# Kernel optimization log

Measured on AMD Instinct MI355X. Metric: run time of the kernel, lower is better.

Reference implementation:

```python
import jax, jax.numpy as jnp
import numpy as np

N = 50000   # nodes
E = 600000  # directed edges (self-loops added inside reference, per GCNConv default)
G = 64      # graphs in the batch
D = 128     # in_features
H = 128     # hidden_channels
C = 10      # num_classes


def setup_inputs() -> dict:
    key = jax.random.key(0)
    ks = jax.random.split(key, 9)
    x = jax.random.normal(ks[0], (N, D), dtype=jnp.float32)
    edge_index = jax.random.randint(ks[1], (2, E), 0, N, dtype=jnp.int64)
    batch = jnp.sort(jax.random.randint(ks[2], (N,), 0, G, dtype=jnp.int64))
    # GCNConv weights (glorot-ish scale) and biases; final linear layer
    W1 = jax.random.normal(ks[3], (D, H), dtype=jnp.float32) / np.sqrt(D).astype(np.float32)
    b1 = jnp.zeros((H,), dtype=jnp.float32)
    W2 = jax.random.normal(ks[4], (H, H), dtype=jnp.float32) / np.sqrt(H).astype(np.float32)
    b2 = jnp.zeros((H,), dtype=jnp.float32)
    Wlin = jax.random.normal(ks[5], (H, C), dtype=jnp.float32) / np.sqrt(H).astype(np.float32)
    blin = jnp.zeros((C,), dtype=jnp.float32)
    return {"x": x, "W1": W1, "b1": b1, "W2": W2, "b2": b2,
            "Wlin": Wlin, "blin": blin, "edge_index": edge_index, "batch": batch}


def _gcn_conv(x, W, b, row, col, norm):
    # x' = D^{-1/2}(A+I)D^{-1/2} (x W) + b ; aggregate messages from row (src) into col (dst)
    h = x @ W                                   # [N, H] dense GEMM
    msg = norm[:, None] * h[row]                # gather by source index [E+N, H]
    out = jax.ops.segment_sum(msg, col, num_segments=N)  # scatter-add to targets
    return out + b


def reference(x, W1, b1, W2, b2, Wlin, blin, edge_index, batch):
    loops = jnp.arange(N, dtype=edge_index.dtype)
    row = jnp.concatenate([edge_index[0], loops])   # sources (+ self loops)
    col = jnp.concatenate([edge_index[1], loops])   # targets (+ self loops)
    # symmetric degree normalization (degrees >= 1 thanks to self loops)
    deg = jax.ops.segment_sum(jnp.ones_like(col, dtype=jnp.float32), col, num_segments=N)
    dinv = jax.lax.rsqrt(deg)
    norm = dinv[row] * dinv[col]                    # [E+N]

    h = jax.nn.relu(_gcn_conv(x, W1, b1, row, col, norm))
    h = _gcn_conv(h, W2, b2, row, col, norm)

    # global mean pool over graphs
    sums = jax.ops.segment_sum(h, batch, num_segments=G)                       # [G, H]
    cnt = jax.ops.segment_sum(jnp.ones((N,), dtype=jnp.float32), batch, num_segments=G)
    pooled = sums / jnp.maximum(cnt, 1.0)[:, None]

    return pooled @ Wlin + blin                     # logits [G, C]
```

## Files before the change

kernel.cpp:

```cpp
#include <hip/hip_runtime.h>

#define NN 50000
#define NE 600000
#define NG 64
#define DIM 128
#define NCLS 10
#define SB 196
#define NNP 50176
#define KBLK 224
#define KCH 224
#define CAP 64
#define E2B ((NE / 2 + 255) / 256)

typedef unsigned short ushort;
typedef unsigned char uchar;
typedef __attribute__((ext_vector_type(8))) short short8;
typedef __attribute__((ext_vector_type(4))) float float4v;
typedef __attribute__((ext_vector_type(2))) float float2v;

__device__ __forceinline__ ushort f2bf(float f) {
    unsigned u = __float_as_uint(f);
    u += 0x7fff + ((u >> 16) & 1);
    return (ushort)(u >> 16);
}
__device__ __forceinline__ uchar f2fp8(float f) {
    int p = __builtin_amdgcn_cvt_pk_fp8_f32(f, f, 0, false);
    return (uchar)(p & 0xff);
}
__device__ __forceinline__ void accfp8(float* a, uint2 v) {
    float2v p0 = __builtin_amdgcn_cvt_pk_f32_fp8(v.x, false);
    float2v p1 = __builtin_amdgcn_cvt_pk_f32_fp8(v.x, true);
    float2v p2 = __builtin_amdgcn_cvt_pk_f32_fp8(v.y, false);
    float2v p3 = __builtin_amdgcn_cvt_pk_f32_fp8(v.y, true);
    a[0] += p0[0]; a[1] += p0[1]; a[2] += p1[0]; a[3] += p1[1];
    a[4] += p2[0]; a[5] += p2[1]; a[6] += p3[0]; a[7] += p3[1];
}

__global__ void k_init(int* __restrict__ cnt, const float* __restrict__ W1,
                       ushort* __restrict__ Wsw, float* __restrict__ Wd) {
    int b = blockIdx.x, t = threadIdx.x;
    if (b < SB) {
        int i = b * 256 + t;
        if (i < NN) cnt[i] = 0;
    } else if (b < SB + 64) {
        int tid = (b - SB) * 256 + t;
        int j = tid & 7;
        int lane = (tid >> 3) & 63;
        int frag = tid >> 9;
        int nt = frag >> 2, kc = frag & 3;
        int k = kc * 32 + (lane >> 4) * 8 + j;
        int n = nt * 16 + (lane & 15);
        Wsw[tid] = f2bf(W1[k * DIM + n]);
    } else {
        float4* w4 = (float4*)Wd;
        int base = (b - SB - 64) * 256 + t;
#pragma unroll
        for (int i = 0; i < 4; ++i)
            w4[base + i * 200704] = make_float4(0.f, 0.f, 0.f, 0.f);
    }
}

__global__ void k_fill(const int* __restrict__ row, const int* __restrict__ col,
                       int* __restrict__ cnt, int* __restrict__ ell) {
    int e = (blockIdx.x * blockDim.x + threadIdx.x) * 2;
    if (e < NE) {
        int2 r = *(const int2*)(row + e);
        int2 c = *(const int2*)(col + e);
        int p0 = atomicAdd(&cnt[c.x], 1);
        if (p0 < CAP) ell[c.x * CAP + p0] = r.x;
        int p1 = atomicAdd(&cnt[c.y], 1);
        if (p1 < CAP) ell[c.y * CAP + p1] = r.y;
    }
}

__global__ __launch_bounds__(256) void k_gemm_mfma(const float* __restrict__ Ain,
                                                   const ushort* __restrict__ Wsw,
                                                   const int* __restrict__ cnt,
                                                   uchar* __restrict__ Hs,
                                                   float* __restrict__ dinv) {
    const int t = threadIdx.x;
    const int wave = t >> 6, lane = t & 63;
    const int m = lane & 15, quad = lane >> 4;
    const int row0 = blockIdx.x * 64 + wave * 16;

    short8 bfrag[8][4];
#pragma unroll
    for (int nt = 0; nt < 8; ++nt)
#pragma unroll
        for (int kc = 0; kc < 4; ++kc)
            bfrag[nt][kc] = *(const short8*)(Wsw + ((nt * 4 + kc) * 64 + lane) * 8);

    float4v acc[8];
#pragma unroll
    for (int nt = 0; nt < 8; ++nt) acc[nt] = (float4v){0.f, 0.f, 0.f, 0.f};

    const int row = row0 + m;
    const int rclamp = row < NN ? row : NN - 1;

#pragma unroll
    for (int kc = 0; kc < 4; ++kc) {
        const float* ap = Ain + (size_t)rclamp * DIM + kc * 32 + quad * 8;
        float4 v0 = *(const float4*)ap;
        float4 v1 = *(const float4*)(ap + 4);
        union { short8 v; ushort u[8]; } tmp;
        tmp.u[0] = f2bf(v0.x); tmp.u[1] = f2bf(v0.y);
        tmp.u[2] = f2bf(v0.z); tmp.u[3] = f2bf(v0.w);
        tmp.u[4] = f2bf(v1.x); tmp.u[5] = f2bf(v1.y);
        tmp.u[6] = f2bf(v1.z); tmp.u[7] = f2bf(v1.w);
        short8 a = tmp.v;
#pragma unroll
        for (int nt = 0; nt < 8; ++nt)
            acc[nt] = __builtin_amdgcn_mfma_f32_16x16x32_bf16(a, bfrag[nt][kc], acc[nt], 0, 0, 0);
    }

#pragma unroll
    for (int reg = 0; reg < 4; ++reg) {
        int r = row0 + quad * 4 + reg;
        if (r < NN) {
            float d = rsqrtf(1.0f + (float)cnt[r]);
            if (m == 0) dinv[r] = d;
#pragma unroll
            for (int nt = 0; nt < 8; ++nt)
                Hs[(size_t)r * DIM + nt * 16 + m] = f2fp8(d * acc[nt][reg]);
        }
    }
}

__global__ __launch_bounds__(256) void k_gather_ell(const int* __restrict__ ell,
                                                    const int* __restrict__ deg,
                                                    const float* __restrict__ bias,
                                                    const uchar* __restrict__ Hs,
                                                    ushort* __restrict__ out) {
    int gt = blockIdx.x * blockDim.x + threadIdx.x;
    int node = gt >> 4, lane = gt & 15;
    if (node >= NN) return;
    const int* rowp = ell + node * CAP;
    int end = min(deg[node], CAP);
    const size_t off = (size_t)lane * 8;

    float a[8] = {0.f, 0.f, 0.f, 0.f, 0.f, 0.f, 0.f, 0.f};
    accfp8(a, *(const uint2*)(Hs + (size_t)node * DIM + off));

    int e = 0;
    for (; e + 8 <= end; e += 8) {
        int r0 = rowp[e], r1 = rowp[e + 1], r2 = rowp[e + 2], r3 = rowp[e + 3];
        int r4 = rowp[e + 4], r5 = rowp[e + 5], r6 = rowp[e + 6], r7 = rowp[e + 7];
        uint2 v0 = *(const uint2*)(Hs + (size_t)r0 * DIM + off);
        uint2 v1 = *(const uint2*)(Hs + (size_t)r1 * DIM + off);
        uint2 v2 = *(const uint2*)(Hs + (size_t)r2 * DIM + off);
        uint2 v3 = *(const uint2*)(Hs + (size_t)r3 * DIM + off);
        uint2 v4 = *(const uint2*)(Hs + (size_t)r4 * DIM + off);
        uint2 v5 = *(const uint2*)(Hs + (size_t)r5 * DIM + off);
        uint2 v6 = *(const uint2*)(Hs + (size_t)r6 * DIM + off);
        uint2 v7 = *(const uint2*)(Hs + (size_t)r7 * DIM + off);
        accfp8(a, v0); accfp8(a, v1); accfp8(a, v2); accfp8(a, v3);
        accfp8(a, v4); accfp8(a, v5); accfp8(a, v6); accfp8(a, v7);
    }
    for (; e + 4 <= end; e += 4) {
        int r0 = rowp[e], r1 = rowp[e + 1], r2 = rowp[e + 2], r3 = rowp[e + 3];
        uint2 v0 = *(const uint2*)(Hs + (size_t)r0 * DIM + off);
        uint2 v1 = *(const uint2*)(Hs + (size_t)r1 * DIM + off);
        uint2 v2 = *(const uint2*)(Hs + (size_t)r2 * DIM + off);
        uint2 v3 = *(const uint2*)(Hs + (size_t)r3 * DIM + off);
        accfp8(a, v0); accfp8(a, v1); accfp8(a, v2); accfp8(a, v3);
    }
    for (; e < end; ++e)
        accfp8(a, *(const uint2*)(Hs + (size_t)rowp[e] * DIM + off));

    float d = rsqrtf(1.0f + (float)end);
    float4 b0 = *(const float4*)(bias + off);
    float4 b1 = *(const float4*)(bias + off + 4);
    a[0] = fmaxf(fmaf(a[0], d, b0.x), 0.f); a[1] = fmaxf(fmaf(a[1], d, b0.y), 0.f);
    a[2] = fmaxf(fmaf(a[2], d, b0.z), 0.f); a[3] = fmaxf(fmaf(a[3], d, b0.w), 0.f);
    a[4] = fmaxf(fmaf(a[4], d, b1.x), 0.f); a[5] = fmaxf(fmaf(a[5], d, b1.y), 0.f);
    a[6] = fmaxf(fmaf(a[6], d, b1.z), 0.f); a[7] = fmaxf(fmaf(a[7], d, b1.w), 0.f);
    uint4 o;
    o.x = (unsigned)f2bf(a[0]) | ((unsigned)f2bf(a[1]) << 16);
    o.y = (unsigned)f2bf(a[2]) | ((unsigned)f2bf(a[3]) << 16);
    o.z = (unsigned)f2bf(a[4]) | ((unsigned)f2bf(a[5]) << 16);
    o.w = (unsigned)f2bf(a[6]) | ((unsigned)f2bf(a[7]) << 16);
    *(uint4*)(out + (size_t)node * DIM + off) = o;
}

__global__ void k_wbuild(const int* __restrict__ row, const int* __restrict__ col,
                         const float* __restrict__ dinv, const int* __restrict__ batch,
                         float* __restrict__ Wd) {
    int b = blockIdx.x, t = threadIdx.x;
    if (b < E2B) {
        int e = (b * 256 + t) * 2;
        if (e < NE) {
            int2 r = *(const int2*)(row + e);
            int2 c = *(const int2*)(col + e);
            atomicAdd(&Wd[(size_t)batch[c.x] * NNP + r.x], dinv[c.x] * dinv[r.x]);
            atomicAdd(&Wd[(size_t)batch[c.y] * NNP + r.y], dinv[c.y] * dinv[r.y]);
        }
    } else {
        int n = (b - E2B) * 256 + t;
        if (n < NN) {
            float d = dinv[n];
            atomicAdd(&Wd[(size_t)batch[n] * NNP + n], d * d);
        }
    }
}

__global__ __launch_bounds__(256) void k_pool_gemm(const float* __restrict__ Wd,
                                                   const ushort* __restrict__ A2,
                                                   float* __restrict__ partial) {
    const int t = threadIdx.x;
    const int wave = t >> 6, lane = t & 63;
    const int m = lane & 15, quad = lane >> 4;
    const int g = wave * 16 + m;
    const size_t k0 = (size_t)blockIdx.x * KCH;

    float4v acc[8];
#pragma unroll
    for (int nt = 0; nt < 8; ++nt) acc[nt] = (float4v){0.f, 0.f, 0.f, 0.f};

    for (int ks = 0; ks < KCH; ks += 32) {
        const size_t kb = k0 + ks + quad * 8;
        const float* ap = Wd + (size_t)g * NNP + kb;
        float4 a0 = *(const float4*)ap;
        float4 a1 = *(const float4*)(ap + 4);
        union { short8 v; ushort u[8]; } af;
        af.u[0] = f2bf(a0.x); af.u[1] = f2bf(a0.y);
        af.u[2] = f2bf(a0.z); af.u[3] = f2bf(a0.w);
        af.u[4] = f2bf(a1.x); af.u[5] = f2bf(a1.y);
        af.u[6] = f2bf(a1.z); af.u[7] = f2bf(a1.w);

        const ushort* bbase = A2 + kb * DIM + m;
#pragma unroll
        for (int nt = 0; nt < 8; ++nt) {
            union { short8 v; ushort u[8]; } bf;
            const ushort* bp = bbase + nt * 16;
#pragma unroll
            for (int j = 0; j < 8; ++j) bf.u[j] = bp[(size_t)j * DIM];
            acc[nt] = __builtin_amdgcn_mfma_f32_16x16x32_bf16(af.v, bf.v, acc[nt], 0, 0, 0);
        }
    }

    float* dst = partial + (size_t)blockIdx.x * (NG * DIM);
#pragma unroll
    for (int reg = 0; reg < 4; ++reg) {
        int gg = wave * 16 + quad * 4 + reg;
#pragma unroll
        for (int nt = 0; nt < 8; ++nt)
            dst[gg * DIM + nt * 16 + m] = acc[nt][reg];
    }
}

__global__ __launch_bounds__(128) void k_final(const float* __restrict__ partial,
                                               const float* __restrict__ W2,
                                               const float* __restrict__ b2,
                                               const float* __restrict__ Wlin,
                                               const float* __restrict__ blin,
                                               const int* __restrict__ batch,
                                               float* __restrict__ out) {
    const int g = blockIdx.x;
    const int t = threadIdx.x;
    int start;
    { int a = 0, b = NN; while (a < b) { int m = (a + b) >> 1; if (batch[m] < g) a = m + 1; else b = m; } start = a; }
    int end;
    { int a = 0, b = NN; while (a < b) { int m = (a + b) >> 1; if (batch[m] < g + 1) a = m + 1; else b = m; } end = a; }
    const int cnt = end - start;

    float s = 0.f;
    for (int b = 0; b < KBLK; b += 4) {
        float s0 = partial[(size_t)(b + 0) * (NG * DIM) + g * DIM + t];
        float s1 = partial[(size_t)(b + 1) * (NG * DIM) + g * DIM + t];
        float s2 = partial[(size_t)(b + 2) * (NG * DIM) + g * DIM + t];
        float s3 = partial[(size_t)(b + 3) * (NG * DIM) + g * DIM + t];
        s += (s0 + s1) + (s2 + s3);
    }
    __shared__ float P[DIM];
    P[t] = s;
    __syncthreads();
    float acc = 0.f;
    for (int k = 0; k < DIM; ++k) acc += P[k] * W2[k * DIM + t];
    __shared__ float pooled[DIM];
    pooled[t] = (cnt > 0) ? (acc / (float)cnt + b2[t]) : 0.f;
    __syncthreads();
    if (t < NCLS) {
        float s2 = blin[t];
        for (int k = 0; k < DIM; ++k) s2 += pooled[k] * Wlin[k * NCLS + t];
        out[g * NCLS + t] = s2;
    }
}

extern "C" void kernel_launch(void* const* d_in, const int* in_sizes, int n_in,
                              void* d_out, int out_size, void* d_ws, size_t ws_size,
                              hipStream_t stream) {
    const float* x    = (const float*)d_in[0];
    const float* W1   = (const float*)d_in[1];
    const float* b1   = (const float*)d_in[2];
    const float* W2   = (const float*)d_in[3];
    const float* b2   = (const float*)d_in[4];
    const float* Wlin = (const float*)d_in[5];
    const float* blin = (const float*)d_in[6];
    const int* eidx   = (const int*)d_in[7];
    const int* batch  = (const int*)d_in[8];
    float* out = (float*)d_out;

    char* ws = (char*)d_ws;
    int*    cnt   = (int*)(ws + 0);
    float*  dinv  = (float*)(ws + 200000);
    int*    ell   = (int*)(ws + 400000);
    ushort* Wsw   = (ushort*)(ws + 13200000);
    float*  Wd    = (float*)(ws + 13232768);
    uchar*  Hs1   = (uchar*)(ws + 26077824);
    ushort* bufB  = (ushort*)(ws + 32477824);
    float*  poolpt= (float*)(ws + 45322880);

    const int* erow = eidx;
    const int* ecol = eidx + NE;

    k_init<<<SB + 64 + 784, 256, 0, stream>>>(cnt, W1, Wsw, Wd);
    k_fill<<<E2B, 256, 0, stream>>>(erow, ecol, cnt, ell);

    const int gemm_grid = (NN + 63) / 64;
    const int node_grid = (NN * 16 + 255) / 256;

    k_gemm_mfma<<<gemm_grid, 256, 0, stream>>>(x, Wsw, cnt, Hs1, dinv);
    k_gather_ell<<<node_grid, 256, 0, stream>>>(ell, cnt, b1, Hs1, bufB);

    k_wbuild<<<E2B + SB, 256, 0, stream>>>(erow, ecol, dinv, batch, Wd);
    k_pool_gemm<<<KBLK, 256, 0, stream>>>(Wd, bufB, poolpt);

    k_final<<<NG, 128, 0, stream>>>(poolpt, W2, b2, Wlin, blin, batch, out);
}
```

Measured before the change: 210.4 us.

## Fuse pooling weight matrix build into layer-1 gather, factoring out source dinv

Drops the separate edge-scan kernel that built the graph-to-node pooling weight matrix with atomics. The layer-1 ELL gather now adds the destination dinv into T[batch[node]][src] as it walks each node's neighbours. The source-side dinv factor is applied later, when k_pool_gemm loads the matrix. This saves one kernel launch and a second pass over the edge list and batch/dinv gathers, but adds atomics inside the gather loop. It also pads dinv with zeros and shifts the workspace offsets to fit.

```diff
diff --git a/kernel.cpp b/kernel.cpp
--- a/kernel.cpp
+++ b/kernel.cpp
@@ -37,7 +37,8 @@
 }
 
 __global__ void k_init(int* __restrict__ cnt, const float* __restrict__ W1,
-                       ushort* __restrict__ Wsw, float* __restrict__ Wd) {
+                       ushort* __restrict__ Wsw, float* __restrict__ T,
+                       float* __restrict__ dinv) {
     int b = blockIdx.x, t = threadIdx.x;
     if (b < SB) {
         int i = b * 256 + t;
@@ -51,12 +52,14 @@
         int k = kc * 32 + (lane >> 4) * 8 + j;
         int n = nt * 16 + (lane & 15);
         Wsw[tid] = f2bf(W1[k * DIM + n]);
-    } else {
-        float4* w4 = (float4*)Wd;
+    } else if (b < SB + 64 + 784) {
+        float4* w4 = (float4*)T;
         int base = (b - SB - 64) * 256 + t;
 #pragma unroll
         for (int i = 0; i < 4; ++i)
             w4[base + i * 200704] = make_float4(0.f, 0.f, 0.f, 0.f);
+    } else {
+        if (t < NNP - NN) dinv[NN + t] = 0.f;
     }
 }
 
@@ -128,23 +131,29 @@
 
 __global__ __launch_bounds__(256) void k_gather_ell(const int* __restrict__ ell,
                                                     const int* __restrict__ deg,
+                                                    const int* __restrict__ batch,
                                                     const float* __restrict__ bias,
                                                     const uchar* __restrict__ Hs,
+                                                    float* __restrict__ T,
                                                     ushort* __restrict__ out) {
     int gt = blockIdx.x * blockDim.x + threadIdx.x;
     int node = gt >> 4, lane = gt & 15;
     if (node >= NN) return;
     const int* rowp = ell + node * CAP;
     int end = min(deg[node], CAP);
+    const float d = rsqrtf(1.0f + (float)end);
+    float* Trow = T + (size_t)batch[node] * NNP;
     const size_t off = (size_t)lane * 8;
 
     float a[8] = {0.f, 0.f, 0.f, 0.f, 0.f, 0.f, 0.f, 0.f};
     accfp8(a, *(const uint2*)(Hs + (size_t)node * DIM + off));
+    if (lane == 0) atomicAdd(&Trow[node], d);
 
     int e = 0;
     for (; e + 8 <= end; e += 8) {
         int r0 = rowp[e], r1 = rowp[e + 1], r2 = rowp[e + 2], r3 = rowp[e + 3];
         int r4 = rowp[e + 4], r5 = rowp[e + 5], r6 = rowp[e + 6], r7 = rowp[e + 7];
+        if (lane < 8) atomicAdd(&Trow[rowp[e + lane]], d);
         uint2 v0 = *(const uint2*)(Hs + (size_t)r0 * DIM + off);
         uint2 v1 = *(const uint2*)(Hs + (size_t)r1 * DIM + off);
         uint2 v2 = *(const uint2*)(Hs + (size_t)r2 * DIM + off);
@@ -158,16 +167,19 @@
     }
     for (; e + 4 <= end; e += 4) {
         int r0 = rowp[e], r1 = rowp[e + 1], r2 = rowp[e + 2], r3 = rowp[e + 3];
+        if (lane < 4) atomicAdd(&Trow[rowp[e + lane]], d);
         uint2 v0 = *(const uint2*)(Hs + (size_t)r0 * DIM + off);
         uint2 v1 = *(const uint2*)(Hs + (size_t)r1 * DIM + off);
         uint2 v2 = *(const uint2*)(Hs + (size_t)r2 * DIM + off);
         uint2 v3 = *(const uint2*)(Hs + (size_t)r3 * DIM + off);
         accfp8(a, v0); accfp8(a, v1); accfp8(a, v2); accfp8(a, v3);
     }
-    for (; e < end; ++e)
-        accfp8(a, *(const uint2*)(Hs + (size_t)rowp[e] * DIM + off));
-
-    float d = rsqrtf(1.0f + (float)end);
+    for (; e < end; ++e) {
+        int r = rowp[e];
+        if (lane == 0) atomicAdd(&Trow[r], d);
+        accfp8(a, *(const uint2*)(Hs + (size_t)r * DIM + off));
+    }
+
     float4 b0 = *(const float4*)(bias + off);
     float4 b1 = *(const float4*)(bias + off + 4);
     a[0] = fmaxf(fmaf(a[0], d, b0.x), 0.f); a[1] = fmaxf(fmaf(a[1], d, b0.y), 0.f);
@@ -182,28 +194,8 @@
     *(uint4*)(out + (size_t)node * DIM + off) = o;
 }
 
-__global__ void k_wbuild(const int* __restrict__ row, const int* __restrict__ col,
-                         const float* __restrict__ dinv, const int* __restrict__ batch,
-                         float* __restrict__ Wd) {
-    int b = blockIdx.x, t = threadIdx.x;
-    if (b < E2B) {
-        int e = (b * 256 + t) * 2;
-        if (e < NE) {
-            int2 r = *(const int2*)(row + e);
-            int2 c = *(const int2*)(col + e);
-            atomicAdd(&Wd[(size_t)batch[c.x] * NNP + r.x], dinv[c.x] * dinv[r.x]);
-            atomicAdd(&Wd[(size_t)batch[c.y] * NNP + r.y], dinv[c.y] * dinv[r.y]);
-        }
-    } else {
-        int n = (b - E2B) * 256 + t;
-        if (n < NN) {
-            float d = dinv[n];
-            atomicAdd(&Wd[(size_t)batch[n] * NNP + n], d * d);
-        }
-    }
-}
-
-__global__ __launch_bounds__(256) void k_pool_gemm(const float* __restrict__ Wd,
+__global__ __launch_bounds__(256) void k_pool_gemm(const float* __restrict__ T,
+                                                   const float* __restrict__ dinv,
                                                    const ushort* __restrict__ A2,
                                                    float* __restrict__ partial) {
     const int t = threadIdx.x;
@@ -218,14 +210,16 @@
 
     for (int ks = 0; ks < KCH; ks += 32) {
         const size_t kb = k0 + ks + quad * 8;
-        const float* ap = Wd + (size_t)g * NNP + kb;
+        const float* ap = T + (size_t)g * NNP + kb;
         float4 a0 = *(const float4*)ap;
         float4 a1 = *(const float4*)(ap + 4);
+        float4 d0 = *(const float4*)(dinv + kb);
+        float4 d1 = *(const float4*)(dinv + kb + 4);
         union { short8 v; ushort u[8]; } af;
-        af.u[0] = f2bf(a0.x); af.u[1] = f2bf(a0.y);
-        af.u[2] = f2bf(a0.z); af.u[3] = f2bf(a0.w);
-        af.u[4] = f2bf(a1.x); af.u[5] = f2bf(a1.y);
-        af.u[6] = f2bf(a1.z); af.u[7] = f2bf(a1.w);
+        af.u[0] = f2bf(a0.x * d0.x); af.u[1] = f2bf(a0.y * d0.y);
+        af.u[2] = f2bf(a0.z * d0.z); af.u[3] = f2bf(a0.w * d0.w);
+        af.u[4] = f2bf(a1.x * d1.x); af.u[5] = f2bf(a1.y * d1.y);
+        af.u[6] = f2bf(a1.z * d1.z); af.u[7] = f2bf(a1.w * d1.w);
 
         const ushort* bbase = A2 + kb * DIM + m;
 #pragma unroll
@@ -303,27 +297,26 @@
     char* ws = (char*)d_ws;
     int*    cnt   = (int*)(ws + 0);
     float*  dinv  = (float*)(ws + 200000);
-    int*    ell   = (int*)(ws + 400000);
-    ushort* Wsw   = (ushort*)(ws + 13200000);
-    float*  Wd    = (float*)(ws + 13232768);
-    uchar*  Hs1   = (uchar*)(ws + 26077824);
-    ushort* bufB  = (ushort*)(ws + 32477824);
-    float*  poolpt= (float*)(ws + 45322880);
+    int*    ell   = (int*)(ws + 400704);
+    ushort* Wsw   = (ushort*)(ws + 13200704);
+    float*  T     = (float*)(ws + 13233472);
+    uchar*  Hs1   = (uchar*)(ws + 26078528);
+    ushort* bufB  = (ushort*)(ws + 32478528);
+    float*  poolpt= (float*)(ws + 45323584);
 
     const int* erow = eidx;
     const int* ecol = eidx + NE;
 
-    k_init<<<SB + 64 + 784, 256, 0, stream>>>(cnt, W1, Wsw, Wd);
+    k_init<<<SB + 64 + 784 + 1, 256, 0, stream>>>(cnt, W1, Wsw, T, dinv);
     k_fill<<<E2B, 256, 0, stream>>>(erow, ecol, cnt, ell);
 
     const int gemm_grid = (NN + 63) / 64;
     const int node_grid = (NN * 16 + 255) / 256;
 
     k_gemm_mfma<<<gemm_grid, 256, 0, stream>>>(x, Wsw, cnt, Hs1, dinv);
-    k_gather_ell<<<node_grid, 256, 0, stream>>>(ell, cnt, b1, Hs1, bufB);
-
-    k_wbuild<<<E2B + SB, 256, 0, stream>>>(erow, ecol, dinv, batch, Wd);
-    k_pool_gemm<<<KBLK, 256, 0, stream>>>(Wd, bufB, poolpt);
+    k_gather_ell<<<node_grid, 256, 0, stream>>>(ell, cnt, batch, b1, Hs1, T, bufB);
+
+    k_pool_gemm<<<KBLK, 256, 0, stream>>>(T, dinv, bufB, poolpt);
 
     k_final<<<NG, 128, 0, stream>>>(poolpt, W2, b2, Wlin, blin, batch, out);
 }
```

Result: faster. 204.0 us, median of 2 (-3.1%).
